# Performance work log

Hardware: AMD Instinct MI355X
Metric: run time of the kernel (lower is better)

The kernel has to match this reference:

```python
import math
import jax, jax.numpy as jnp
from jax import lax
import numpy as np

D_MODEL, D_STATE, D_CONV, EXPAND = 96, 16, 3, 2
D_INNER = EXPAND * D_MODEL            # 192
DT_RANK = math.ceil(D_MODEL / 16)     # 6
B_, H_, W_ = 2, 64, 64


def setup_inputs() -> dict:
    key = jax.random.key(0)
    ks = jax.random.split(key, 8)
    x = jax.random.normal(ks[0], (B_, H_, W_, D_MODEL), jnp.float32)
    in_proj_w = jax.random.normal(ks[1], (2 * D_INNER, D_MODEL), jnp.float32) * (D_MODEL ** -0.5)
    conv_w = jax.random.normal(ks[2], (D_INNER, 1, D_CONV, D_CONV), jnp.float32) * 0.1  # depthwise OIHW
    conv_b = jax.random.normal(ks[3], (D_INNER,), jnp.float32) * 0.1
    x_proj_weight = jax.random.normal(ks[4], (4, DT_RANK + 2 * D_STATE, D_INNER), jnp.float32) * (D_INNER ** -0.5)
    dt_init_std = DT_RANK ** -0.5
    dt_projs_weight = jax.random.uniform(ks[5], (4, D_INNER, DT_RANK), jnp.float32, -dt_init_std, dt_init_std)
    dt = jnp.exp(jax.random.uniform(ks[6], (4, D_INNER), jnp.float32) * (math.log(0.1) - math.log(0.001)) + math.log(0.001))
    dt = jnp.clip(dt, 1e-4, None)
    dt_projs_bias = dt + jnp.log(-jnp.expm1(-dt))  # inverse softplus init
    A_logs = jnp.log(jnp.tile(jnp.arange(1.0, D_STATE + 1.0, dtype=jnp.float32), (4 * D_INNER, 1)))  # (4*D, N)
    Ds = jnp.ones((4 * D_INNER,), jnp.float32)
    out_norm_w = jnp.ones((D_INNER,), jnp.float32)
    out_norm_b = jnp.zeros((D_INNER,), jnp.float32)
    out_proj_w = jax.random.normal(ks[7], (D_MODEL, D_INNER), jnp.float32) * (D_INNER ** -0.5)
    return dict(x=x, in_proj_w=in_proj_w, conv_w=conv_w, conv_b=conv_b,
                x_proj_weight=x_proj_weight, dt_projs_weight=dt_projs_weight,
                dt_projs_bias=dt_projs_bias, A_logs=A_logs, Ds=Ds,
                out_norm_w=out_norm_w, out_norm_b=out_norm_b, out_proj_w=out_proj_w)


def _ss2d(x, in_proj_w, conv_w, conv_b, x_proj_weight, dt_projs_weight,
          dt_projs_bias, A_logs, Ds, out_norm_w, out_norm_b, out_proj_w):
    B, H, W, C = x.shape
    K = 4
    d_inner = conv_w.shape[0]
    d_state = A_logs.shape[1]
    dt_rank = dt_projs_weight.shape[2]
    L = H * W

    # in_proj + split into x / gate z
    xz = jnp.einsum('bhwc,ec->bhwe', x, in_proj_w)
    xi, z = jnp.split(xz, 2, axis=-1)

    # depthwise 3x3 conv (padding=1) + SiLU, channels-first
    xc = jnp.transpose(xi, (0, 3, 1, 2))  # B,D,H,W
    xc = lax.conv_general_dilated(xc, conv_w, (1, 1), 'SAME',
                                  feature_group_count=d_inner,
                                  dimension_numbers=('NCHW', 'OIHW', 'NCHW'))
    xc = jax.nn.silu(xc + conv_b[None, :, None, None])

    # 4 scan directions: row-major, col-major, and their reverses
    x_hw = xc.reshape(B, d_inner, L)
    x_wh = jnp.transpose(xc, (0, 1, 3, 2)).reshape(B, d_inner, L)
    x_hwwh = jnp.stack([x_hw, x_wh], axis=1)                        # B,2,D,L
    xs = jnp.concatenate([x_hwwh, jnp.flip(x_hwwh, axis=-1)], axis=1)  # B,K,D,L

    x_dbl = jnp.einsum('bkdl,kcd->bkcl', xs, x_proj_weight)
    dts, Bs, Cs = jnp.split(x_dbl, [dt_rank, dt_rank + d_state], axis=2)
    dts = jnp.einsum('bkrl,kdr->bkdl', dts, dt_projs_weight)
    delta = jax.nn.softplus(dts + dt_projs_bias[None, :, :, None])  # B,K,D,L
    A = -jnp.exp(A_logs).reshape(K, d_inner, d_state)               # K,D,N

    # selective scan over L (serial recurrence)
    d_s = jnp.moveaxis(delta, -1, 0)  # L,B,K,D
    u_s = jnp.moveaxis(xs, -1, 0)     # L,B,K,D
    B_s = jnp.moveaxis(Bs, -1, 0)     # L,B,K,N
    C_s = jnp.moveaxis(Cs, -1, 0)     # L,B,K,N

    def step(h, inp):
        d_t, u_t, Bt, Ct = inp
        dA = jnp.exp(d_t[..., None] * A)                       # B,K,D,N
        h = h * dA + (d_t * u_t)[..., None] * Bt[:, :, None, :]
        y = jnp.einsum('bkdn,bkn->bkd', h, Ct)
        return h, y

    h0 = jnp.zeros((B, K, d_inner, d_state), jnp.float32)
    _, ys = lax.scan(step, h0, (d_s, u_s, B_s, C_s))  # ys: L,B,K,D
    ys = jnp.moveaxis(ys, 0, -1)                      # B,K,D,L
    out_y = ys + xs * Ds.reshape(K, d_inner)[None, :, :, None]

    # merge directions back to row-major layout
    inv_y = jnp.flip(out_y[:, 2:4], axis=-1)
    wh_y = jnp.transpose(out_y[:, 1].reshape(B, d_inner, W, H), (0, 1, 3, 2)).reshape(B, d_inner, L)
    invwh_y = jnp.transpose(inv_y[:, 1].reshape(B, d_inner, W, H), (0, 1, 3, 2)).reshape(B, d_inner, L)
    y = out_y[:, 0] + inv_y[:, 0] + wh_y + invwh_y    # B,D,L

    y = jnp.transpose(y, (0, 2, 1)).reshape(B, H, W, d_inner)
    mu = y.mean(-1, keepdims=True)
    var = y.var(-1, keepdims=True)
    y = (y - mu) * lax.rsqrt(var + 1e-5) * out_norm_w + out_norm_b
    y = y * jax.nn.silu(z)
    return jnp.einsum('bhwd,cd->bhwc', y, out_proj_w)


def reference(x, in_proj_w, conv_w, conv_b, x_proj_weight, dt_projs_weight,
              dt_projs_bias, A_logs, Ds, out_norm_w, out_norm_b, out_proj_w):
    return _ss2d(x, in_proj_w, conv_w, conv_b, x_proj_weight, dt_projs_weight,
                 dt_projs_bias, A_logs, Ds, out_norm_w, out_norm_b, out_proj_w)
```

## Files before the change

kernel.cpp:

```cpp
#include <hip/hip_runtime.h>
#include <math.h>

#define DMODEL 96
#define DIN    192
#define NST    16
#define RK     6
#define KDIR   4
#define LLEN   4096
#define BB     2
#define BP_TOT 8192
#define SCH    128
#define TCH    32

__global__ __launch_bounds__(192) void k_inproj(const float* __restrict__ x,
                                                const float* __restrict__ Wp,
                                                float* __restrict__ xi,
                                                float* __restrict__ z)
{
    __shared__ float xs[8 * 96];
    const int t  = threadIdx.x;
    const int p0 = blockIdx.x * 8;
    #pragma unroll
    for (int idx = t; idx < 768; idx += 192)
        xs[idx] = x[(size_t)p0 * 96 + idx];
    __syncthreads();

    float acc0[8], acc1[8];
    #pragma unroll
    for (int i = 0; i < 8; ++i) { acc0[i] = 0.f; acc1[i] = 0.f; }
    const float* w0p = Wp + (size_t)t * 96;
    const float* w1p = Wp + (size_t)(t + 192) * 96;
    for (int k = 0; k < 96; k += 4) {
        float4 w0 = *(const float4*)(w0p + k);
        float4 w1 = *(const float4*)(w1p + k);
        #pragma unroll
        for (int p = 0; p < 8; ++p) {
            float4 xv = *(const float4*)&xs[p * 96 + k];
            acc0[p] = fmaf(w0.x, xv.x, fmaf(w0.y, xv.y, fmaf(w0.z, xv.z, fmaf(w0.w, xv.w, acc0[p]))));
            acc1[p] = fmaf(w1.x, xv.x, fmaf(w1.y, xv.y, fmaf(w1.z, xv.z, fmaf(w1.w, xv.w, acc1[p]))));
        }
    }
    #pragma unroll
    for (int p = 0; p < 8; ++p) {
        xi[(size_t)(p0 + p) * 192 + t] = acc0[p];
        z [(size_t)(p0 + p) * 192 + t] = acc1[p];
    }
}

__global__ __launch_bounds__(256) void k_conv(const float* __restrict__ xi,
                                              const float* __restrict__ cw,
                                              const float* __restrict__ cb,
                                              float* __restrict__ xc)
{
    int tid = blockIdx.x * 256 + threadIdx.x;
    int d  = tid % 192;
    int bp = tid / 192;
    int p  = bp & 4095;
    int b  = bp >> 12;
    int h  = p >> 6, w = p & 63;
    float s = cb[d];
    #pragma unroll
    for (int ky = 0; ky < 3; ++ky) {
        int hh = h + ky - 1;
        if (hh < 0 || hh >= 64) continue;
        #pragma unroll
        for (int kx = 0; kx < 3; ++kx) {
            int ww = w + kx - 1;
            if (ww < 0 || ww >= 64) continue;
            s += xi[((size_t)b * 4096 + hh * 64 + ww) * 192 + d] * cw[d * 9 + ky * 3 + kx];
        }
    }
    xc[tid] = s * (1.f / (1.f + __expf(-s)));
}

__device__ __forceinline__ int inv_perm(int kd, int p)
{
    if (kd == 0) return p;
    if (kd == 1) return ((p & 63) << 6) | (p >> 6);
    if (kd == 2) return 4095 - p;
    return 4095 - (((p & 63) << 6) | (p >> 6));
}

__device__ __forceinline__ int perm_pos(int k, int l)
{
    if (k == 0) return l;
    if (k == 1) return ((l & 63) << 6) | (l >> 6);
    if (k == 2) return 4095 - l;
    int lr = 4095 - l;
    return ((lr & 63) << 6) | (lr >> 6);
}

__global__ __launch_bounds__(192) void k_xdbl(const float* __restrict__ xc,
                                              const float* __restrict__ xpw,
                                              float* __restrict__ xdk)
{
    __shared__ float xs[8 * 192];
    const int t  = threadIdx.x;
    const int p0 = blockIdx.x * 8;
    #pragma unroll
    for (int idx = t; idx < 1536; idx += 192)
        xs[idx] = xc[(size_t)p0 * 192 + idx];
    __syncthreads();
    if (t >= 152) return;

    const int kd = t / 38, r = t % 38;
    float acc[8];
    #pragma unroll
    for (int i = 0; i < 8; ++i) acc[i] = 0.f;
    const float* wr = xpw + (size_t)t * 192;
    for (int k = 0; k < 192; k += 4) {
        float4 w = *(const float4*)(wr + k);
        #pragma unroll
        for (int p = 0; p < 8; ++p) {
            float4 xv = *(const float4*)&xs[p * 192 + k];
            acc[p] = fmaf(w.x, xv.x, fmaf(w.y, xv.y, fmaf(w.z, xv.z, fmaf(w.w, xv.w, acc[p]))));
        }
    }
    #pragma unroll
    for (int p = 0; p < 8; ++p) {
        int bp = p0 + p;
        int b  = bp >> 12, pp = bp & 4095;
        int l  = inv_perm(kd, pp);
        xdk[((size_t)(b * 4 + kd) * 4096 + l) * 38 + r] = acc[p];
    }
}

__device__ __forceinline__ float softplus_fast(float x)
{
    float r = __logf(1.f + __expf(x));
    return (x > 15.f) ? x : r;
}

__device__ __forceinline__ void pow_chain(float e1, float* aa)
{
    float e2 = e1 * e1, e4 = e2 * e2, e8 = e4 * e4, e16 = e8 * e8;
    float e3 = e2 * e1, e5 = e4 * e1, e6 = e4 * e2, e7 = e4 * e3;
    aa[0] = e1;  aa[1] = e2;  aa[2] = e3;  aa[3] = e4;
    aa[4] = e5;  aa[5] = e6;  aa[6] = e7;  aa[7] = e8;
    aa[8] = e8 * e1;  aa[9] = e8 * e2;  aa[10] = e8 * e3;  aa[11] = e8 * e4;
    aa[12] = e8 * e5; aa[13] = e8 * e6; aa[14] = e8 * e7;  aa[15] = e16;
}

__device__ __forceinline__ int sm_remap(int c)
{
    return (c < 6) ? (32 + c) : (c - 6);
}

__global__ __launch_bounds__(192) void k_scan1(const float* __restrict__ xc,
                                               const float* __restrict__ xdk,
                                               const float* __restrict__ dtw,
                                               const float* __restrict__ dtb,
                                               const float* __restrict__ Alog,
                                               float* __restrict__ hend,
                                               float* __restrict__ prodA)
{
    __shared__ float sm[TCH * 40];
    const int t   = threadIdx.x;
    const int blk = blockIdx.x;
    const int s = blk & (SCH - 1), k = (blk >> 7) & 3, b = blk >> 9;
    const int kd = k * 192 + t;
    const int l0 = s * TCH;

    const float* src = xdk + ((size_t)(b * 4 + k) * 4096 + l0) * 38;
    #pragma unroll
    for (int idx = t; idx < TCH * 38; idx += 192) {
        int st = idx / 38, c = idx % 38;
        sm[st * 40 + sm_remap(c)] = src[idx];
    }

    const float A0 = -__expf(Alog[kd * 16]);
    bool fast = true;
    #pragma unroll
    for (int n = 1; n < 16; ++n) {
        float An = -__expf(Alog[kd * 16 + n]);
        fast = fast && (fabsf(An - (float)(n + 1) * A0) <= 1e-3f * fabsf(An));
    }
    float wdt[6];
    #pragma unroll
    for (int r = 0; r < 6; ++r) wdt[r] = dtw[kd * 6 + r];
    const float bias = dtb[kd];

    float h[16];
    #pragma unroll
    for (int n = 0; n < 16; ++n) h[n] = 0.f;
    float cd = 0.f;

    const float* xcb = xc + (size_t)b * 4096 * 192;
    int allfast = __syncthreads_and((int)fast);

    int p_cur = perm_pos(k, l0);
    float u = xcb[(size_t)p_cur * 192 + t];

    if (allfast) {
        for (int st = 0; st < TCH; ++st) {
            int p_next = (st + 1 < TCH) ? perm_pos(k, l0 + st + 1) : p_cur;
            float u_next = xcb[(size_t)p_next * 192 + t];
            const float* r = &sm[st * 40];
            float4 dq = *(const float4*)(r + 32);
            float xv = bias + dq.x * wdt[0] + dq.y * wdt[1] + dq.z * wdt[2]
                            + dq.w * wdt[3] + r[36] * wdt[4] + r[37] * wdt[5];
            float delta = softplus_fast(xv);
            cd += delta;
            float du = delta * u;
            float aa[16];
            pow_chain(__expf(delta * A0), aa);
            float4 b0 = *(const float4*)(r),      b1 = *(const float4*)(r + 4);
            float4 b2 = *(const float4*)(r + 8),  b3 = *(const float4*)(r + 12);
            float bv[16] = {b0.x, b0.y, b0.z, b0.w, b1.x, b1.y, b1.z, b1.w,
                            b2.x, b2.y, b2.z, b2.w, b3.x, b3.y, b3.z, b3.w};
            #pragma unroll
            for (int n = 0; n < 16; ++n) h[n] = fmaf(h[n], aa[n], du * bv[n]);
            u = u_next; p_cur = p_next;
        }
    } else {
        for (int st = 0; st < TCH; ++st) {
            int p_next = (st + 1 < TCH) ? perm_pos(k, l0 + st + 1) : p_cur;
            float u_next = xcb[(size_t)p_next * 192 + t];
            const float* r = &sm[st * 40];
            float xv = bias;
            #pragma unroll
            for (int j = 0; j < 6; ++j) xv += r[32 + j] * wdt[j];
            float delta = softplus_fast(xv);
            cd += delta;
            float du = delta * u;
            #pragma unroll
            for (int n = 0; n < 16; ++n) {
                float An = -__expf(Alog[kd * 16 + n]);
                h[n] = fmaf(h[n], __expf(delta * An), du * r[n]);
            }
            u = u_next; p_cur = p_next;
        }
    }

    size_t base = (size_t)blk * 3072 + t * 16;
    float ap[16];
    if (allfast) {
        pow_chain(__expf(cd * A0), ap);
    } else {
        #pragma unroll
        for (int n = 0; n < 16; ++n)
            ap[n] = __expf(-__expf(Alog[kd * 16 + n]) * cd);
    }
    #pragma unroll
    for (int i = 0; i < 4; ++i) {
        *(float4*)&hend [base + 4 * i] = make_float4(h[4*i], h[4*i+1], h[4*i+2], h[4*i+3]);
        *(float4*)&prodA[base + 4 * i] = make_float4(ap[4*i], ap[4*i+1], ap[4*i+2], ap[4*i+3]);
    }
}

__global__ __launch_bounds__(256) void k_scan2(const float* __restrict__ hend,
                                               float* __restrict__ prodA)
{
    int tid = blockIdx.x * 256 + threadIdx.x;
    int n  = tid & 15;
    int d  = (tid >> 4) % 192;
    int bk = tid / (192 * 16);
    size_t base = (size_t)bk * SCH * 3072 + d * 16 + n;
    float carry = 0.f;
    for (int s = 0; s < SCH; ++s) {
        size_t a = base + (size_t)s * 3072;
        float pa = prodA[a];
        float he = hend[a];
        prodA[a] = carry;
        carry = fmaf(pa, carry, he);
    }
}

__global__ __launch_bounds__(192) void k_scan3(const float* __restrict__ xc,
                                               const float* __restrict__ xdk,
                                               const float* __restrict__ dtw,
                                               const float* __restrict__ dtb,
                                               const float* __restrict__ Alog,
                                               const float* __restrict__ Ds,
                                               const float* __restrict__ hinit,
                                               float* __restrict__ y)
{
    __shared__ float sm[TCH * 40];
    const int t   = threadIdx.x;
    const int blk = blockIdx.x;
    const int s = blk & (SCH - 1), k = (blk >> 7) & 3, b = blk >> 9;
    const int kd = k * 192 + t;
    const int l0 = s * TCH;

    const float* src = xdk + ((size_t)(b * 4 + k) * 4096 + l0) * 38;
    #pragma unroll
    for (int idx = t; idx < TCH * 38; idx += 192) {
        int st = idx / 38, c = idx % 38;
        sm[st * 40 + sm_remap(c)] = src[idx];
    }

    const float A0 = -__expf(Alog[kd * 16]);
    bool fast = true;
    #pragma unroll
    for (int n = 1; n < 16; ++n) {
        float An = -__expf(Alog[kd * 16 + n]);
        fast = fast && (fabsf(An - (float)(n + 1) * A0) <= 1e-3f * fabsf(An));
    }
    float wdt[6];
    #pragma unroll
    for (int r = 0; r < 6; ++r) wdt[r] = dtw[kd * 6 + r];
    const float bias = dtb[kd];
    const float Dk   = Ds[kd];

    float h[16];
    size_t hbase = (size_t)blk * 3072 + t * 16;
    #pragma unroll
    for (int i = 0; i < 4; ++i) {
        float4 v = *(const float4*)&hinit[hbase + 4 * i];
        h[4*i] = v.x; h[4*i+1] = v.y; h[4*i+2] = v.z; h[4*i+3] = v.w;
    }

    const float* xcb = xc + (size_t)b * 4096 * 192;
    float* yb = y + (size_t)b * 4096 * 192;
    int allfast = __syncthreads_and((int)fast);

    int p_cur = perm_pos(k, l0);
    float u = xcb[(size_t)p_cur * 192 + t];

    if (allfast) {
        for (int st = 0; st < TCH; ++st) {
            int p_next = (st + 1 < TCH) ? perm_pos(k, l0 + st + 1) : p_cur;
            float u_next = xcb[(size_t)p_next * 192 + t];
            const float* r = &sm[st * 40];
            float4 dq = *(const float4*)(r + 32);
            float xv = bias + dq.x * wdt[0] + dq.y * wdt[1] + dq.z * wdt[2]
                            + dq.w * wdt[3] + r[36] * wdt[4] + r[37] * wdt[5];
            float delta = softplus_fast(xv);
            float du = delta * u;
            float aa[16];
            pow_chain(__expf(delta * A0), aa);
            float4 b0 = *(const float4*)(r),      b1 = *(const float4*)(r + 4);
            float4 b2 = *(const float4*)(r + 8),  b3 = *(const float4*)(r + 12);
            float4 c0 = *(const float4*)(r + 16), c1 = *(const float4*)(r + 20);
            float4 c2 = *(const float4*)(r + 24), c3 = *(const float4*)(r + 28);
            float bv[16] = {b0.x, b0.y, b0.z, b0.w, b1.x, b1.y, b1.z, b1.w,
                            b2.x, b2.y, b2.z, b2.w, b3.x, b3.y, b3.z, b3.w};
            float cv[16] = {c0.x, c0.y, c0.z, c0.w, c1.x, c1.y, c1.z, c1.w,
                            c2.x, c2.y, c2.z, c2.w, c3.x, c3.y, c3.z, c3.w};
            float acc = Dk * u;
            #pragma unroll
            for (int n = 0; n < 16; ++n) {
                h[n] = fmaf(h[n], aa[n], du * bv[n]);
                acc  = fmaf(h[n], cv[n], acc);
            }
            unsafeAtomicAdd(&yb[(size_t)p_cur * 192 + t], acc);
            u = u_next; p_cur = p_next;
        }
    } else {
        for (int st = 0; st < TCH; ++st) {
            int p_next = (st + 1 < TCH) ? perm_pos(k, l0 + st + 1) : p_cur;
            float u_next = xcb[(size_t)p_next * 192 + t];
            const float* r = &sm[st * 40];
            float xv = bias;
            #pragma unroll
            for (int j = 0; j < 6; ++j) xv += r[32 + j] * wdt[j];
            float delta = softplus_fast(xv);
            float du = delta * u;
            float acc = Dk * u;
            #pragma unroll
            for (int n = 0; n < 16; ++n) {
                float An = -__expf(Alog[kd * 16 + n]);
                h[n] = fmaf(h[n], __expf(delta * An), du * r[n]);
                acc  = fmaf(h[n], r[16 + n], acc);
            }
            unsafeAtomicAdd(&yb[(size_t)p_cur * 192 + t], acc);
            u = u_next; p_cur = p_next;
        }
    }
}

__global__ __launch_bounds__(192) void k_lngate(const float* __restrict__ y,
                                                const float* __restrict__ z,
                                                const float* __restrict__ onw,
                                                const float* __restrict__ onb,
                                                float* __restrict__ yg)
{
    const int t  = threadIdx.x;
    const int bp = blockIdx.x;
    float yv = y[(size_t)bp * 192 + t];
    float s1 = yv, s2 = yv * yv;
    #pragma unroll
    for (int off = 32; off; off >>= 1) {
        s1 += __shfl_xor(s1, off, 64);
        s2 += __shfl_xor(s2, off, 64);
    }
    __shared__ float rs[3], rq[3];
    int wv = t >> 6;
    if ((t & 63) == 0) { rs[wv] = s1; rq[wv] = s2; }
    __syncthreads();
    float tot  = rs[0] + rs[1] + rs[2];
    float totq = rq[0] + rq[1] + rq[2];
    float mean = tot * (1.f / 192.f);
    float var  = totq * (1.f / 192.f) - mean * mean;
    float rinv = rsqrtf(var + 1e-5f);
    float yn = (yv - mean) * rinv * onw[t] + onb[t];
    float zv = z[(size_t)bp * 192 + t];
    float sig = 1.f / (1.f + __expf(-zv));
    yg[(size_t)bp * 192 + t] = yn * (zv * sig);
}

__global__ __launch_bounds__(192) void k_outproj(const float* __restrict__ yg,
                                                 const float* __restrict__ Wo,
                                                 float* __restrict__ out)
{
    __shared__ float ys[8 * 192];
    const int t  = threadIdx.x;
    const int p0 = blockIdx.x * 8;
    #pragma unroll
    for (int idx = t; idx < 1536; idx += 192)
        ys[idx] = yg[(size_t)p0 * 192 + idx];
    __syncthreads();

    const int pg = t / 96, c = t % 96;
    float acc[4];
    #pragma unroll
    for (int i = 0; i < 4; ++i) acc[i] = 0.f;
    const float* wr = Wo + (size_t)c * 192;
    for (int k = 0; k < 192; k += 4) {
        float4 w = *(const float4*)(wr + k);
        #pragma unroll
        for (int i = 0; i < 4; ++i) {
            float4 xv = *(const float4*)&ys[(pg * 4 + i) * 192 + k];
            acc[i] = fmaf(w.x, xv.x, fmaf(w.y, xv.y, fmaf(w.z, xv.z, fmaf(w.w, xv.w, acc[i]))));
        }
    }
    #pragma unroll
    for (int i = 0; i < 4; ++i)
        out[(size_t)(p0 + pg * 4 + i) * 96 + c] = acc[i];
}

extern "C" void kernel_launch(void* const* d_in, const int* in_sizes, int n_in,
                              void* d_out, int out_size, void* d_ws, size_t ws_size,
                              hipStream_t stream)
{
    const float* x    = (const float*)d_in[0];
    const float* Wp   = (const float*)d_in[1];
    const float* cw   = (const float*)d_in[2];
    const float* cb   = (const float*)d_in[3];
    const float* xpw  = (const float*)d_in[4];
    const float* dtw  = (const float*)d_in[5];
    const float* dtb  = (const float*)d_in[6];
    const float* Alog = (const float*)d_in[7];
    const float* Ds   = (const float*)d_in[8];
    const float* onw  = (const float*)d_in[9];
    const float* onb  = (const float*)d_in[10];
    const float* Wo   = (const float*)d_in[11];
    float* out = (float*)d_out;

    const size_t NBP  = (size_t)BP_TOT * 192;
    const size_t NXD  = (size_t)BB * 4 * 4096 * 38;
    const size_t NSC  = (size_t)BB * 4 * SCH * 3072;
    float* WS    = (float*)d_ws;
    float* xc    = WS;
    float* zb    = WS + NBP;
    float* xiy   = WS + 2 * NBP;
    float* xdk   = WS + 3 * NBP;
    float* hend  = xdk + NXD;
    float* prodA = hend + NSC;
    float* yg    = hend;

    k_inproj <<<1024, 192, 0, stream>>>(x, Wp, xiy, zb);
    k_conv   <<<6144, 256, 0, stream>>>(xiy, cw, cb, xc);
    hipMemsetAsync(xiy, 0, NBP * sizeof(float), stream);
    k_xdbl   <<<1024, 192, 0, stream>>>(xc, xpw, xdk);
    k_scan1  <<<1024, 192, 0, stream>>>(xc, xdk, dtw, dtb, Alog, hend, prodA);
    k_scan2  <<<96, 256, 0, stream>>>(hend, prodA);
    k_scan3  <<<1024, 192, 0, stream>>>(xc, xdk, dtw, dtb, Alog, Ds, prodA, xiy);
    k_lngate <<<8192, 192, 0, stream>>>(xiy, zb, onw, onb, yg);
    k_outproj<<<1024, 192, 0, stream>>>(yg, Wo, out);
}
```

Baseline: 231.2 us.

## Emit local scan outputs in pass one; make pass three a carry-in correction

Pass one of the chunked selective scan now computes the zero-initial-state outputs directly, including the C projection and D skip, and atomically adds them into y. It also stores cumulative delta per step. Pass three, on the fast path, only adds the correction term exp(cumdelta*A)*h_init dotted with C, using the stored cumulative deltas, and returns early for the first chunk. This avoids recomputing softplus, the B terms and the input reads. Separately, the y zeroing is folded into the xdbl kernel and LayerNorm+gate is fused into the output projection. Together these remove a memset and a launch, at the cost of an extra cumulative-delta buffer write and atomics split across two passes.

```diff
diff --git a/kernel.cpp b/kernel.cpp
--- a/kernel.cpp
+++ b/kernel.cpp
@@ -20,7 +20,6 @@
     __shared__ float xs[8 * 96];
     const int t  = threadIdx.x;
     const int p0 = blockIdx.x * 8;
-    #pragma unroll
     for (int idx = t; idx < 768; idx += 192)
         xs[idx] = x[(size_t)p0 * 96 + idx];
     __syncthreads();
@@ -90,41 +89,6 @@
     return ((lr & 63) << 6) | (lr >> 6);
 }
 
-__global__ __launch_bounds__(192) void k_xdbl(const float* __restrict__ xc,
-                                              const float* __restrict__ xpw,
-                                              float* __restrict__ xdk)
-{
-    __shared__ float xs[8 * 192];
-    const int t  = threadIdx.x;
-    const int p0 = blockIdx.x * 8;
-    #pragma unroll
-    for (int idx = t; idx < 1536; idx += 192)
-        xs[idx] = xc[(size_t)p0 * 192 + idx];
-    __syncthreads();
-    if (t >= 152) return;
-
-    const int kd = t / 38, r = t % 38;
-    float acc[8];
-    #pragma unroll
-    for (int i = 0; i < 8; ++i) acc[i] = 0.f;
-    const float* wr = xpw + (size_t)t * 192;
-    for (int k = 0; k < 192; k += 4) {
-        float4 w = *(const float4*)(wr + k);
-        #pragma unroll
-        for (int p = 0; p < 8; ++p) {
-            float4 xv = *(const float4*)&xs[p * 192 + k];
-            acc[p] = fmaf(w.x, xv.x, fmaf(w.y, xv.y, fmaf(w.z, xv.z, fmaf(w.w, xv.w, acc[p]))));
-        }
-    }
-    #pragma unroll
-    for (int p = 0; p < 8; ++p) {
-        int bp = p0 + p;
-        int b  = bp >> 12, pp = bp & 4095;
-        int l  = inv_perm(kd, pp);
-        xdk[((size_t)(b * 4 + kd) * 4096 + l) * 38 + r] = acc[p];
-    }
-}
-
 __device__ __forceinline__ float softplus_fast(float x)
 {
     float r = __logf(1.f + __expf(x));
@@ -146,13 +110,53 @@
     return (c < 6) ? (32 + c) : (c - 6);
 }
 
+__global__ __launch_bounds__(192) void k_xdbl(const float* __restrict__ xc,
+                                              const float* __restrict__ xpw,
+                                              float* __restrict__ xdk,
+                                              float* __restrict__ y)
+{
+    __shared__ float xs[8 * 192];
+    const int t  = threadIdx.x;
+    const int p0 = blockIdx.x * 8;
+    for (int idx = t; idx < 1536; idx += 192) {
+        xs[idx] = xc[(size_t)p0 * 192 + idx];
+        y[(size_t)p0 * 192 + idx] = 0.f;
+    }
+    __syncthreads();
+    if (t >= 152) return;
+
+    const int kd = t / 38, r = t % 38;
+    float acc[8];
+    #pragma unroll
+    for (int i = 0; i < 8; ++i) acc[i] = 0.f;
+    const float* wr = xpw + (size_t)t * 192;
+    for (int k = 0; k < 192; k += 4) {
+        float4 w = *(const float4*)(wr + k);
+        #pragma unroll
+        for (int p = 0; p < 8; ++p) {
+            float4 xv = *(const float4*)&xs[p * 192 + k];
+            acc[p] = fmaf(w.x, xv.x, fmaf(w.y, xv.y, fmaf(w.z, xv.z, fmaf(w.w, xv.w, acc[p]))));
+        }
+    }
+    #pragma unroll
+    for (int p = 0; p < 8; ++p) {
+        int bp = p0 + p;
+        int b  = bp >> 12, pp = bp & 4095;
+        int l  = inv_perm(kd, pp);
+        xdk[((size_t)(b * 4 + kd) * 4096 + l) * 38 + r] = acc[p];
+    }
+}
+
 __global__ __launch_bounds__(192) void k_scan1(const float* __restrict__ xc,
                                                const float* __restrict__ xdk,
                                                const float* __restrict__ dtw,
                                                const float* __restrict__ dtb,
                                                const float* __restrict__ Alog,
+                                               const float* __restrict__ Ds,
                                                float* __restrict__ hend,
-                                               float* __restrict__ prodA)
+                                               float* __restrict__ prodA,
+                                               float* __restrict__ cdbuf,
+                                               float* __restrict__ y)
 {
     __shared__ float sm[TCH * 40];
     const int t   = threadIdx.x;
@@ -162,7 +166,6 @@
     const int l0 = s * TCH;
 
     const float* src = xdk + ((size_t)(b * 4 + k) * 4096 + l0) * 38;
-    #pragma unroll
     for (int idx = t; idx < TCH * 38; idx += 192) {
         int st = idx / 38, c = idx % 38;
         sm[st * 40 + sm_remap(c)] = src[idx];
@@ -179,6 +182,7 @@
     #pragma unroll
     for (int r = 0; r < 6; ++r) wdt[r] = dtw[kd * 6 + r];
     const float bias = dtb[kd];
+    const float Dk   = Ds[kd];
 
     float h[16];
     #pragma unroll
@@ -186,6 +190,7 @@
     float cd = 0.f;
 
     const float* xcb = xc + (size_t)b * 4096 * 192;
+    float* yb = y + (size_t)b * 4096 * 192;
     int allfast = __syncthreads_and((int)fast);
 
     int p_cur = perm_pos(k, l0);
@@ -201,15 +206,25 @@
                             + dq.w * wdt[3] + r[36] * wdt[4] + r[37] * wdt[5];
             float delta = softplus_fast(xv);
             cd += delta;
+            cdbuf[((size_t)blk * TCH + st) * 192 + t] = cd;
             float du = delta * u;
             float aa[16];
             pow_chain(__expf(delta * A0), aa);
             float4 b0 = *(const float4*)(r),      b1 = *(const float4*)(r + 4);
             float4 b2 = *(const float4*)(r + 8),  b3 = *(const float4*)(r + 12);
+            float4 c0 = *(const float4*)(r + 16), c1 = *(const float4*)(r + 20);
+            float4 c2 = *(const float4*)(r + 24), c3 = *(const float4*)(r + 28);
             float bv[16] = {b0.x, b0.y, b0.z, b0.w, b1.x, b1.y, b1.z, b1.w,
                             b2.x, b2.y, b2.z, b2.w, b3.x, b3.y, b3.z, b3.w};
-            #pragma unroll
-            for (int n = 0; n < 16; ++n) h[n] = fmaf(h[n], aa[n], du * bv[n]);
+            float cv[16] = {c0.x, c0.y, c0.z, c0.w, c1.x, c1.y, c1.z, c1.w,
+                            c2.x, c2.y, c2.z, c2.w, c3.x, c3.y, c3.z, c3.w};
+            float acc = Dk * u;
+            #pragma unroll
+            for (int n = 0; n < 16; ++n) {
+                h[n] = fmaf(h[n], aa[n], du * bv[n]);
+                acc  = fmaf(h[n], cv[n], acc);
+            }
+            unsafeAtomicAdd(&yb[(size_t)p_cur * 192 + t], acc);
             u = u_next; p_cur = p_next;
         }
     } else {
@@ -273,6 +288,7 @@
                                                const float* __restrict__ Alog,
                                                const float* __restrict__ Ds,
                                                const float* __restrict__ hinit,
+                                               const float* __restrict__ cdbuf,
                                                float* __restrict__ y)
 {
     __shared__ float sm[TCH * 40];
@@ -283,11 +299,7 @@
     const int l0 = s * TCH;
 
     const float* src = xdk + ((size_t)(b * 4 + k) * 4096 + l0) * 38;
-    #pragma unroll
-    for (int idx = t; idx < TCH * 38; idx += 192) {
-        int st = idx / 38, c = idx % 38;
-        sm[st * 40 + sm_remap(c)] = src[idx];
-    }
+    float* yb = y + (size_t)b * 4096 * 192;
 
     const float A0 = -__expf(Alog[kd * 16]);
     bool fast = true;
@@ -296,57 +308,54 @@
         float An = -__expf(Alog[kd * 16 + n]);
         fast = fast && (fabsf(An - (float)(n + 1) * A0) <= 1e-3f * fabsf(An));
     }
-    float wdt[6];
-    #pragma unroll
-    for (int r = 0; r < 6; ++r) wdt[r] = dtw[kd * 6 + r];
-    const float bias = dtb[kd];
-    const float Dk   = Ds[kd];
-
-    float h[16];
+    int allfast = __syncthreads_and((int)fast);
+
+    float hi[16];
     size_t hbase = (size_t)blk * 3072 + t * 16;
     #pragma unroll
     for (int i = 0; i < 4; ++i) {
         float4 v = *(const float4*)&hinit[hbase + 4 * i];
-        h[4*i] = v.x; h[4*i+1] = v.y; h[4*i+2] = v.z; h[4*i+3] = v.w;
-    }
-
-    const float* xcb = xc + (size_t)b * 4096 * 192;
-    float* yb = y + (size_t)b * 4096 * 192;
-    int allfast = __syncthreads_and((int)fast);
-
-    int p_cur = perm_pos(k, l0);
-    float u = xcb[(size_t)p_cur * 192 + t];
+        hi[4*i] = v.x; hi[4*i+1] = v.y; hi[4*i+2] = v.z; hi[4*i+3] = v.w;
+    }
 
     if (allfast) {
+        if (s == 0) return;
+        for (int idx = t; idx < TCH * 16; idx += 192) {
+            int st = idx >> 4, c = idx & 15;
+            sm[st * 16 + c] = src[st * 38 + 22 + c];
+        }
+        __syncthreads();
+        const float* cdp = cdbuf + (size_t)blk * TCH * 192 + t;
+        float cd_next = cdp[0];
         for (int st = 0; st < TCH; ++st) {
-            int p_next = (st + 1 < TCH) ? perm_pos(k, l0 + st + 1) : p_cur;
-            float u_next = xcb[(size_t)p_next * 192 + t];
-            const float* r = &sm[st * 40];
-            float4 dq = *(const float4*)(r + 32);
-            float xv = bias + dq.x * wdt[0] + dq.y * wdt[1] + dq.z * wdt[2]
-                            + dq.w * wdt[3] + r[36] * wdt[4] + r[37] * wdt[5];
-            float delta = softplus_fast(xv);
-            float du = delta * u;
+            float cdv = cd_next;
+            if (st + 1 < TCH) cd_next = cdp[(size_t)(st + 1) * 192];
             float aa[16];
-            pow_chain(__expf(delta * A0), aa);
-            float4 b0 = *(const float4*)(r),      b1 = *(const float4*)(r + 4);
-            float4 b2 = *(const float4*)(r + 8),  b3 = *(const float4*)(r + 12);
-            float4 c0 = *(const float4*)(r + 16), c1 = *(const float4*)(r + 20);
-            float4 c2 = *(const float4*)(r + 24), c3 = *(const float4*)(r + 28);
-            float bv[16] = {b0.x, b0.y, b0.z, b0.w, b1.x, b1.y, b1.z, b1.w,
-                            b2.x, b2.y, b2.z, b2.w, b3.x, b3.y, b3.z, b3.w};
-            float cv[16] = {c0.x, c0.y, c0.z, c0.w, c1.x, c1.y, c1.z, c1.w,
-                            c2.x, c2.y, c2.z, c2.w, c3.x, c3.y, c3.z, c3.w};
-            float acc = Dk * u;
-            #pragma unroll
-            for (int n = 0; n < 16; ++n) {
-                h[n] = fmaf(h[n], aa[n], du * bv[n]);
-                acc  = fmaf(h[n], cv[n], acc);
-            }
-            unsafeAtomicAdd(&yb[(size_t)p_cur * 192 + t], acc);
-            u = u_next; p_cur = p_next;
+            pow_chain(__expf(cdv * A0), aa);
+            const float* r = &sm[st * 16];
+            float corr = 0.f;
+            #pragma unroll
+            for (int n = 0; n < 16; ++n)
+                corr = fmaf(aa[n] * hi[n], r[n], corr);
+            unsafeAtomicAdd(&yb[(size_t)perm_pos(k, l0 + st) * 192 + t], corr);
         }
     } else {
+        for (int idx = t; idx < TCH * 38; idx += 192) {
+            int st = idx / 38, c = idx % 38;
+            sm[st * 40 + sm_remap(c)] = src[idx];
+        }
+        __syncthreads();
+        const float* xcb = xc + (size_t)b * 4096 * 192;
+        float wdt[6];
+        #pragma unroll
+        for (int r = 0; r < 6; ++r) wdt[r] = dtw[kd * 6 + r];
+        const float bias = dtb[kd];
+        const float Dk   = Ds[kd];
+        float h[16];
+        #pragma unroll
+        for (int n = 0; n < 16; ++n) h[n] = hi[n];
+        int p_cur = perm_pos(k, l0);
+        float u = xcb[(size_t)p_cur * 192 + t];
         for (int st = 0; st < TCH; ++st) {
             int p_next = (st + 1 < TCH) ? perm_pos(k, l0 + st + 1) : p_cur;
             float u_next = xcb[(size_t)p_next * 192 + t];
@@ -369,46 +378,57 @@
     }
 }
 
-__global__ __launch_bounds__(192) void k_lngate(const float* __restrict__ y,
-                                                const float* __restrict__ z,
-                                                const float* __restrict__ onw,
-                                                const float* __restrict__ onb,
-                                                float* __restrict__ yg)
-{
-    const int t  = threadIdx.x;
-    const int bp = blockIdx.x;
-    float yv = y[(size_t)bp * 192 + t];
-    float s1 = yv, s2 = yv * yv;
-    #pragma unroll
-    for (int off = 32; off; off >>= 1) {
-        s1 += __shfl_xor(s1, off, 64);
-        s2 += __shfl_xor(s2, off, 64);
-    }
-    __shared__ float rs[3], rq[3];
-    int wv = t >> 6;
-    if ((t & 63) == 0) { rs[wv] = s1; rq[wv] = s2; }
-    __syncthreads();
-    float tot  = rs[0] + rs[1] + rs[2];
-    float totq = rq[0] + rq[1] + rq[2];
-    float mean = tot * (1.f / 192.f);
-    float var  = totq * (1.f / 192.f) - mean * mean;
-    float rinv = rsqrtf(var + 1e-5f);
-    float yn = (yv - mean) * rinv * onw[t] + onb[t];
-    float zv = z[(size_t)bp * 192 + t];
-    float sig = 1.f / (1.f + __expf(-zv));
-    yg[(size_t)bp * 192 + t] = yn * (zv * sig);
-}
-
-__global__ __launch_bounds__(192) void k_outproj(const float* __restrict__ yg,
-                                                 const float* __restrict__ Wo,
-                                                 float* __restrict__ out)
-{
-    __shared__ float ys[8 * 192];
+__global__ __launch_bounds__(192) void k_lnout(const float* __restrict__ y,
+                                               const float* __restrict__ zb,
+                                               const float* __restrict__ onw,
+                                               const float* __restrict__ onb,
+                                               const float* __restrict__ Wo,
+                                               float* __restrict__ out)
+{
+    __shared__ float ys[1536];
+    __shared__ float ps[192], pq[192];
+    __shared__ float mu[8], ri[8];
     const int t  = threadIdx.x;
     const int p0 = blockIdx.x * 8;
-    #pragma unroll
-    for (int idx = t; idx < 1536; idx += 192)
-        ys[idx] = yg[(size_t)p0 * 192 + idx];
+
+    #pragma unroll
+    for (int i = 0; i < 8; ++i)
+        ys[i * 192 + t] = y[(size_t)p0 * 192 + i * 192 + t];
+    __syncthreads();
+
+    {
+        int pg = t / 24, j = t % 24;
+        float s1 = 0.f, s2 = 0.f;
+        #pragma unroll
+        for (int m = 0; m < 8; ++m) {
+            float v = ys[pg * 192 + j + 24 * m];
+            s1 += v; s2 += v * v;
+        }
+        ps[t] = s1; pq[t] = s2;
+    }
+    __syncthreads();
+    if (t < 8) {
+        float s1 = 0.f, s2 = 0.f;
+        #pragma unroll
+        for (int j = 0; j < 24; ++j) { s1 += ps[t * 24 + j]; s2 += pq[t * 24 + j]; }
+        float mean = s1 * (1.f / 192.f);
+        float var  = s2 * (1.f / 192.f) - mean * mean;
+        mu[t] = mean;
+        ri[t] = rsqrtf(var + 1e-5f);
+    }
+    __syncthreads();
+
+    {
+        float w = onw[t], bo = onb[t];
+        #pragma unroll
+        for (int i = 0; i < 8; ++i) {
+            float v  = ys[i * 192 + t];
+            float yn = (v - mu[i]) * ri[i] * w + bo;
+            float zv = zb[(size_t)(p0 + i) * 192 + t];
+            float sg = 1.f / (1.f + __expf(-zv));
+            ys[i * 192 + t] = yn * (zv * sg);
+        }
+    }
     __syncthreads();
 
     const int pg = t / 96, c = t % 96;
@@ -457,15 +477,13 @@
     float* xdk   = WS + 3 * NBP;
     float* hend  = xdk + NXD;
     float* prodA = hend + NSC;
-    float* yg    = hend;
-
-    k_inproj <<<1024, 192, 0, stream>>>(x, Wp, xiy, zb);
-    k_conv   <<<6144, 256, 0, stream>>>(xiy, cw, cb, xc);
-    hipMemsetAsync(xiy, 0, NBP * sizeof(float), stream);
-    k_xdbl   <<<1024, 192, 0, stream>>>(xc, xpw, xdk);
-    k_scan1  <<<1024, 192, 0, stream>>>(xc, xdk, dtw, dtb, Alog, hend, prodA);
-    k_scan2  <<<96, 256, 0, stream>>>(hend, prodA);
-    k_scan3  <<<1024, 192, 0, stream>>>(xc, xdk, dtw, dtb, Alog, Ds, prodA, xiy);
-    k_lngate <<<8192, 192, 0, stream>>>(xiy, zb, onw, onb, yg);
-    k_outproj<<<1024, 192, 0, stream>>>(yg, Wo, out);
-}
+    float* cdbuf = prodA + NSC;
+
+    k_inproj<<<1024, 192, 0, stream>>>(x, Wp, xiy, zb);
+    k_conv  <<<6144, 256, 0, stream>>>(xiy, cw, cb, xc);
+    k_xdbl  <<<1024, 192, 0, stream>>>(xc, xpw, xdk, xiy);
+    k_scan1 <<<1024, 192, 0, stream>>>(xc, xdk, dtw, dtb, Alog, Ds, hend, prodA, cdbuf, xiy);
+    k_scan2 <<<96, 256, 0, stream>>>(hend, prodA);
+    k_scan3 <<<1024, 192, 0, stream>>>(xc, xdk, dtw, dtb, Alog, Ds, prodA, cdbuf, xiy);
+    k_lnout <<<1024, 192, 0, stream>>>(xiy, zb, onw, onb, Wo, out);
+}
```

Result: no change. 229.3 us (-0.8%).
